# Optimization experiments

Hardware: AMD Instinct MI355X
Metric: run time of the kernel (lower is better)

The kernel has to match this reference:

```python
import jax, jax.numpy as jnp
import numpy as np

B, T, D, H, HS = 4, 1024, 1024, 16, 64  # T == block_size; HS = D // H


def setup_inputs() -> dict:
    key = jax.random.key(0)
    ks = jax.random.split(key, 9)
    s = 0.02
    x = jax.random.normal(ks[0], (B, T, D), dtype=jnp.float32)
    Wk = jax.random.normal(ks[1], (H, D, HS), dtype=jnp.float32) * s
    bk = jax.random.normal(ks[2], (H, HS), dtype=jnp.float32) * s
    Wq = jax.random.normal(ks[3], (H, D, HS), dtype=jnp.float32) * s
    bq = jax.random.normal(ks[4], (H, HS), dtype=jnp.float32) * s
    Wv = jax.random.normal(ks[5], (H, D, HS), dtype=jnp.float32) * s
    bv = jax.random.normal(ks[6], (H, HS), dtype=jnp.float32) * s
    Wp = jax.random.normal(ks[7], (D, D), dtype=jnp.float32) * s
    bp = jax.random.normal(ks[8], (D,), dtype=jnp.float32) * s
    return {"x": x, "Wk": Wk, "bk": bk, "Wq": Wq, "bq": bq,
            "Wv": Wv, "bv": bv, "Wp": Wp, "bp": bp}


def reference(x, Wk, bk, Wq, bq, Wv, bv, Wp, bp):
    Bx, Tx, Dx = x.shape
    # per-head projections, batched over heads: [B,H,T,HS]
    k = jnp.einsum('btd,hde->bhte', x, Wk) + bk[None, :, None, :]
    q = jnp.einsum('btd,hde->bhte', x, Wq) + bq[None, :, None, :]
    v = jnp.einsum('btd,hde->bhte', x, Wv) + bv[None, :, None, :]
    # NOTE: faithful to source: wei = k @ q^T, scaled by C**-0.5 with C=d_model
    scores = jnp.einsum('bhte,bhse->bhts', k, q) * (Dx ** -0.5)
    causal = jnp.tril(jnp.ones((Tx, Tx), dtype=bool))  # tril == 0 masked to -inf
    scores = jnp.where(causal[None, None], scores, -jnp.inf)
    attn = jax.nn.softmax(scores, axis=-1)  # attn_map (dropout is identity in eval)
    out = jnp.einsum('bhts,bhse->bhte', attn, v)
    # concat heads along feature dim (head order preserved)
    out = out.transpose(0, 2, 1, 3).reshape(Bx, Tx, -1)
    out = out @ Wp + bp  # final projection (output dropout identity in eval)
    return (out, attn)
```

## Files before the change

kernel.cpp:

```cpp
#include <hip/hip_runtime.h>
#include <hip/hip_bf16.h>
#include <stdint.h>


using f32x4 = __attribute__((ext_vector_type(4))) float;
using s16x8 = __attribute__((ext_vector_type(8))) short;

#define GLOAD_LDS16(g, l)                                                          \
  __builtin_amdgcn_global_load_lds((const __attribute__((address_space(1))) void*)(g), \
                                   (__attribute__((address_space(3))) void*)(l), 16, 0, 0)

__device__ __forceinline__ unsigned short f2bf(float f) {
  unsigned u = __float_as_uint(f);
  u = (u + 0x7FFFu + ((u >> 16) & 1u)) >> 16;
  return (unsigned short)u;
}

__global__ __launch_bounds__(256) void prep2_kernel(
    const float* __restrict__ x,
    const float* __restrict__ Wk, const float* __restrict__ Wq,
    const float* __restrict__ Wv,
    const float* __restrict__ bk, const float* __restrict__ bq,
    const float* __restrict__ bv,
    const float* __restrict__ Wp,
    unsigned short* __restrict__ xb,
    unsigned short* __restrict__ Wt,
    unsigned short* __restrict__ Wpt,
    float* __restrict__ bqkv) {
  __shared__ float tile[64][65];
  const int bid = blockIdx.x, t = threadIdx.x;

  if (bid < 1024) {
#pragma unroll
    for (int q = 0; q < 4; ++q) {
      int idx = bid * 1024 + q * 256 + t;
      float4 v = ((const float4*)x)[idx];
      ushort4 o;
      o.x = f2bf(v.x); o.y = f2bf(v.y); o.z = f2bf(v.z); o.w = f2bf(v.w);
      ((ushort4*)xb)[idx] = o;
    }
  } else if (bid < 1792) {
    int wb = bid - 1024;
    int p = wb >> 8, rem = wb & 255;
    int h = rem >> 4, dt = rem & 15;
    int d0 = dt * 64;
    const float* Wsrc = (p == 0) ? Wk : (p == 1) ? Wq : Wv;
    const float* src = Wsrc + ((size_t)h * 1024 + d0) * 64;
#pragma unroll
    for (int q = 0; q < 16; ++q) {
      int idx = t + q * 256;
      int dr = idx >> 6, e = idx & 63;
      tile[dr][e] = src[(size_t)dr * 64 + e];
    }
    __syncthreads();
    unsigned short* dst = Wt + ((size_t)p * 1024 + h * 64) * 1024 + d0;
#pragma unroll
    for (int q = 0; q < 16; ++q) {
      int idx = t + q * 256;
      int er = idx >> 6, dc = idx & 63;
      dst[(size_t)er * 1024 + dc] = f2bf(tile[dc][er]);
    }
  } else if (bid < 2048) {
    int wb = bid - 1792;
    int nt = wb >> 4, dt = wb & 15;
    int n0 = nt * 64, d0 = dt * 64;
#pragma unroll
    for (int q = 0; q < 16; ++q) {
      int idx = t + q * 256;
      int dr = idx >> 6, nc = idx & 63;
      tile[dr][nc] = Wp[(size_t)(d0 + dr) * 1024 + n0 + nc];
    }
    __syncthreads();
#pragma unroll
    for (int q = 0; q < 16; ++q) {
      int idx = t + q * 256;
      int er = idx >> 6, dc = idx & 63;
      Wpt[(size_t)(n0 + er) * 1024 + d0 + dc] = f2bf(tile[dc][er]);
    }
  } else {
#pragma unroll
    for (int q = 0; q < 12; ++q) {
      int c = q * 256 + t;
      int p = c >> 10;
      const float* bsrc = (p == 0) ? bk : (p == 1) ? bq : bv;
      bqkv[c] = bsrc[c & 1023];
    }
  }
}

template <int MODE>
__global__ __launch_bounds__(256, 2) void gemm_bt(
    const unsigned short* __restrict__ A,
    const unsigned short* __restrict__ Bt,
    const float* __restrict__ bias,
    unsigned short* __restrict__ kbuf,
    unsigned short* __restrict__ qbuf,
    unsigned short* __restrict__ vtbuf,
    float* __restrict__ fout,
    int gridN) {
  const int K = 1024;
  __shared__ __align__(16) unsigned short As[128 * 64];
  __shared__ __align__(16) unsigned short Bs[128 * 64];

  const int cpx = gridDim.x >> 3;
  const int bid2 = (blockIdx.x & 7) * cpx + (blockIdx.x >> 3);
  const int bm = bid2 / gridN, bn = bid2 % gridN;
  const int tid = threadIdx.x, wave = tid >> 6, lane = tid & 63;
  const int wm = wave >> 1, wn = wave & 1;
  const int l15 = lane & 15, l4 = lane >> 4;
  const long arow0 = (long)bm * 128;
  const long brow0 = (long)bn * 128;

  f32x4 acc[4][4];
  const f32x4 zf4 = {0.f, 0.f, 0.f, 0.f};
#pragma unroll
  for (int i = 0; i < 4; ++i)
#pragma unroll
    for (int j = 0; j < 4; ++j) acc[i][j] = zf4;

  for (int kt = 0; kt < 16; ++kt) {
#pragma unroll
    for (int s = 0; s < 4; ++s) {
      int ob = (wave * 4 + s) * 1024;
      int o = ob + lane * 16;
      int r = o >> 7;
      int cb = (o & 127) ^ ((r & 7) << 4);
      GLOAD_LDS16(A + (arow0 + r) * K + kt * 64 + (cb >> 1), (char*)As + ob);
      GLOAD_LDS16(Bt + (brow0 + r) * K + kt * 64 + (cb >> 1), (char*)Bs + ob);
    }
    __syncthreads();
#pragma unroll
    for (int kk = 0; kk < 2; ++kk) {
      s16x8 af[4], bfv[4];
#pragma unroll
      for (int i = 0; i < 4; ++i) {
        int row = wm * 64 + i * 16 + l15;
        int cb = (kk * 64 + l4 * 16) ^ ((row & 7) << 4);
        af[i] = *(const s16x8*)((const char*)As + row * 128 + cb);
      }
#pragma unroll
      for (int j = 0; j < 4; ++j) {
        int row = wn * 64 + j * 16 + l15;
        int cb = (kk * 64 + l4 * 16) ^ ((row & 7) << 4);
        bfv[j] = *(const s16x8*)((const char*)Bs + row * 128 + cb);
      }
#pragma unroll
      for (int i = 0; i < 4; ++i)
#pragma unroll
        for (int j = 0; j < 4; ++j)
          acc[i][j] = __builtin_amdgcn_mfma_f32_16x16x32_bf16(af[i], bfv[j], acc[i][j], 0, 0, 0);
    }
    __syncthreads();
  }

  const int gc0 = bn * 128;
  if (MODE == 0) {
    const int p = gc0 >> 10;
#pragma unroll
    for (int i = 0; i < 4; ++i) {
      int mrow = (int)arow0 + wm * 64 + i * 16 + l4 * 4;
      int b = mrow >> 10;
      int t = mrow & 1023;
#pragma unroll
      for (int j = 0; j < 4; ++j) {
        int gc = gc0 + wn * 64 + j * 16 + l15;
        int hc = gc & 1023;
        int hh = hc >> 6, e = hc & 63;
        float bb = bias[gc];
#pragma unroll
        for (int r = 0; r < 4; ++r) {
          unsigned short ub = f2bf(acc[i][j][r] + bb);
          if (p == 0)
            kbuf[(((long)(b * 16 + hh)) * 1024 + (t + r)) * 64 + e] = ub;
          else if (p == 1)
            qbuf[(((long)(b * 16 + hh)) * 1024 + (t + r)) * 64 + e] = ub;
          else
            vtbuf[(((long)(b * 16 + hh)) * 64 + e) * 1024 + (t + r)] = ub;
        }
      }
    }
  } else {
#pragma unroll
    for (int i = 0; i < 4; ++i) {
      long mrow = arow0 + wm * 64 + i * 16 + l4 * 4;
#pragma unroll
      for (int j = 0; j < 4; ++j) {
        int gc = gc0 + wn * 64 + j * 16 + l15;
        float bb = bias[gc];
#pragma unroll
        for (int r = 0; r < 4; ++r) fout[(mrow + r) * 1024 + gc] = acc[i][j][r] + bb;
      }
    }
  }
}

__global__ __launch_bounds__(256, 2) void attn_fused(
    const unsigned short* __restrict__ Kb,
    const unsigned short* __restrict__ Qb,
    const unsigned short* __restrict__ Vt,
    float* __restrict__ attn,
    unsigned short* __restrict__ outh) {
  __shared__ __align__(16) unsigned short Ps[128 * 128];
  __shared__ float rsum[2][128];
  __shared__ float rinv[128];

  const int bh = blockIdx.y;
  const int bx = blockIdx.x;
  const int ttile = (bx & 1) ? (7 - (bx >> 1)) : (bx >> 1);
  const int t0 = ttile * 128;
  const int b = bh >> 4, h = bh & 15;
  const unsigned short* Kbh = Kb + (long)bh * 65536;
  const unsigned short* Qbh = Qb + (long)bh * 65536;
  const unsigned short* Vbh = Vt + (long)bh * 65536;
  float* attn_bh = attn + (long)bh * 1048576;

  const int tid = threadIdx.x, wave = tid >> 6, lane = tid & 63;
  const int wm = wave >> 1, wn = wave & 1;
  const int l15 = lane & 15, l4 = lane >> 4;
  const f32x4 zf4 = {0.f, 0.f, 0.f, 0.f};

  s16x8 kf[4][2];
#pragma unroll
  for (int i = 0; i < 4; ++i)
#pragma unroll
    for (int kk = 0; kk < 2; ++kk)
      kf[i][kk] = *(const s16x8*)(Kbh + (long)(t0 + wm * 64 + i * 16 + l15) * 64 + kk * 32 + l4 * 8);

  float rs[4][4];
#pragma unroll
  for (int i = 0; i < 4; ++i)
#pragma unroll
    for (int r = 0; r < 4; ++r) rs[i][r] = 0.f;

  for (int st = 0; st <= ttile; ++st) {
    int s0 = st * 128;
    f32x4 acc[4][4];
#pragma unroll
    for (int i = 0; i < 4; ++i)
#pragma unroll
      for (int j = 0; j < 4; ++j) acc[i][j] = zf4;
#pragma unroll
    for (int kk = 0; kk < 2; ++kk) {
      s16x8 qf[4];
#pragma unroll
      for (int j = 0; j < 4; ++j)
        qf[j] = *(const s16x8*)(Qbh + (long)(s0 + wn * 64 + j * 16 + l15) * 64 + kk * 32 + l4 * 8);
#pragma unroll
      for (int i = 0; i < 4; ++i)
#pragma unroll
        for (int j = 0; j < 4; ++j)
          acc[i][j] = __builtin_amdgcn_mfma_f32_16x16x32_bf16(kf[i][kk], qf[j], acc[i][j], 0, 0, 0);
    }
    bool diag = (st == ttile);
#pragma unroll
    for (int i = 0; i < 4; ++i)
#pragma unroll
      for (int j = 0; j < 4; ++j)
#pragma unroll
        for (int r = 0; r < 4; ++r) {
          float sc = acc[i][j][r] * 0.03125f;
          if (diag) {
            int t = t0 + wm * 64 + i * 16 + l4 * 4 + r;
            int s = s0 + wn * 64 + j * 16 + l15;
            rs[i][r] += (s <= t) ? __expf(sc) : 0.f;
          } else {
            rs[i][r] += __expf(sc);
          }
        }
  }
#pragma unroll
  for (int i = 0; i < 4; ++i)
#pragma unroll
    for (int r = 0; r < 4; ++r) {
      float v = rs[i][r];
      v += __shfl_xor(v, 1);
      v += __shfl_xor(v, 2);
      v += __shfl_xor(v, 4);
      v += __shfl_xor(v, 8);
      if (l15 == 0) rsum[wn][wm * 64 + i * 16 + l4 * 4 + r] = v;
    }
  __syncthreads();
  if (tid < 128) rinv[tid] = 1.0f / (rsum[0][tid] + rsum[1][tid]);
  __syncthreads();

  float rinv_r[4][4];
#pragma unroll
  for (int i = 0; i < 4; ++i)
#pragma unroll
    for (int r = 0; r < 4; ++r) rinv_r[i][r] = rinv[wm * 64 + i * 16 + l4 * 4 + r];

  f32x4 acc2[2][4];
#pragma unroll
  for (int i = 0; i < 2; ++i)
#pragma unroll
    for (int j = 0; j < 4; ++j) acc2[i][j] = zf4;

  for (int st = 0; st < 8; ++st) {
    int s0 = st * 128;
    if (st > ttile) {
      float4 z = make_float4(0.f, 0.f, 0.f, 0.f);
#pragma unroll
      for (int q = 0; q < 16; ++q) {
        int fi = tid + q * 256;
        int row = fi >> 5, c4 = fi & 31;
        *(float4*)(attn_bh + (long)(t0 + row) * 1024 + s0 + c4 * 4) = z;
      }
      continue;
    }
    f32x4 acc[4][4];
#pragma unroll
    for (int i = 0; i < 4; ++i)
#pragma unroll
      for (int j = 0; j < 4; ++j) acc[i][j] = zf4;
#pragma unroll
    for (int kk = 0; kk < 2; ++kk) {
      s16x8 qf[4];
#pragma unroll
      for (int j = 0; j < 4; ++j)
        qf[j] = *(const s16x8*)(Qbh + (long)(s0 + wn * 64 + j * 16 + l15) * 64 + kk * 32 + l4 * 8);
#pragma unroll
      for (int i = 0; i < 4; ++i)
#pragma unroll
        for (int j = 0; j < 4; ++j)
          acc[i][j] = __builtin_amdgcn_mfma_f32_16x16x32_bf16(kf[i][kk], qf[j], acc[i][j], 0, 0, 0);
    }
    bool diag = (st == ttile);
#pragma unroll
    for (int i = 0; i < 4; ++i) {
      int tl = wm * 64 + i * 16 + l4 * 4;
#pragma unroll
      for (int j = 0; j < 4; ++j) {
        int sl = wn * 64 + j * 16 + l15;
#pragma unroll
        for (int r = 0; r < 4; ++r) {
          int t = t0 + tl + r;
          int s = s0 + sl;
          float p = (!diag || s <= t) ? __expf(acc[i][j][r] * 0.03125f) * rinv_r[i][r] : 0.f;
          attn_bh[(long)t * 1024 + s] = p;
          int lt = tl + r;
          Ps[lt * 128 + (sl ^ ((lt & 15) << 3))] = f2bf(p);
        }
      }
    }
    __syncthreads();
#pragma unroll
    for (int kk2 = 0; kk2 < 4; ++kk2) {
      s16x8 pf[2];
#pragma unroll
      for (int i2 = 0; i2 < 2; ++i2) {
        int lt = wave * 32 + i2 * 16 + l15;
        int ls = kk2 * 32 + l4 * 8;
        pf[i2] = *(const s16x8*)&Ps[lt * 128 + (ls ^ ((lt & 15) << 3))];
      }
      s16x8 vf[4];
#pragma unroll
      for (int j2 = 0; j2 < 4; ++j2)
        vf[j2] = *(const s16x8*)(Vbh + (long)(j2 * 16 + l15) * 1024 + s0 + kk2 * 32 + l4 * 8);
#pragma unroll
      for (int i2 = 0; i2 < 2; ++i2)
#pragma unroll
        for (int j2 = 0; j2 < 4; ++j2)
          acc2[i2][j2] = __builtin_amdgcn_mfma_f32_16x16x32_bf16(pf[i2], vf[j2], acc2[i2][j2], 0, 0, 0);
    }
    __syncthreads();
  }

#pragma unroll
  for (int i2 = 0; i2 < 2; ++i2)
#pragma unroll
    for (int j2 = 0; j2 < 4; ++j2)
#pragma unroll
      for (int r = 0; r < 4; ++r) {
        int t = t0 + wave * 32 + i2 * 16 + l4 * 4 + r;
        int e = j2 * 16 + l15;
        outh[(long)(b * 1024 + t) * 1024 + h * 64 + e] = f2bf(acc2[i2][j2][r]);
      }
}

extern "C" void kernel_launch(void* const* d_in, const int* in_sizes, int n_in,
                              void* d_out, int out_size, void* d_ws, size_t ws_size,
                              hipStream_t stream) {
  const float* x  = (const float*)d_in[0];
  const float* Wk = (const float*)d_in[1];
  const float* bk = (const float*)d_in[2];
  const float* Wq = (const float*)d_in[3];
  const float* bq = (const float*)d_in[4];
  const float* Wv = (const float*)d_in[5];
  const float* bv = (const float*)d_in[6];
  const float* Wp = (const float*)d_in[7];
  const float* bp = (const float*)d_in[8];

  char* ws = (char*)d_ws;
  unsigned short* xb   = (unsigned short*)(ws);
  unsigned short* Wt   = (unsigned short*)(ws + 8388608);
  unsigned short* Wpt  = (unsigned short*)(ws + 14680064);
  float*          bqkv = (float*)(ws + 16777216);
  unsigned short* Kbuf = (unsigned short*)(ws + 16789504);
  unsigned short* Qbuf = (unsigned short*)(ws + 25178112);
  unsigned short* Vtb  = (unsigned short*)(ws + 33566720);
  unsigned short* outh = (unsigned short*)(ws + 41955328);

  float* out  = (float*)d_out;
  float* attn = out + 4194304;

  prep2_kernel<<<dim3(2049), dim3(256), 0, stream>>>(x, Wk, Wq, Wv, bk, bq, bv, Wp,
                                                     xb, Wt, Wpt, bqkv);
  gemm_bt<0><<<dim3(768), dim3(256), 0, stream>>>(xb, Wt, bqkv, Kbuf, Qbuf, Vtb,
                                                  (float*)nullptr, 24);
  attn_fused<<<dim3(8, 64), dim3(256), 0, stream>>>(Kbuf, Qbuf, Vtb, attn, outh);
  gemm_bt<1><<<dim3(256), dim3(256), 0, stream>>>(outh, Wpt, bp,
                                                  (unsigned short*)nullptr,
                                                  (unsigned short*)nullptr,
                                                  (unsigned short*)nullptr, out, 8);
}
```

Baseline: 513.4 us.

## Keep full unnormalized probability rows in LDS to avoid recomputing QK in attention

The attention kernel now processes 32-row query tiles and keeps the whole row of exponentiated scores (as bf16) in LDS. This removes the second QK^T pass, which was recomputed only to normalize. The attn matrix is written with coalesced float4 stores scaled by the reciprocal row sum, and normalization of PV is moved to the output. The V projection epilogue also transposes through LDS so that V^T is written with vectorized coalesced stores instead of scattered 2-byte writes. The tradeoff is 64KB of LDS per block, which lowers occupancy. The attn values are also now quantized to bf16 before normalization, which costs some precision.

```diff
diff --git a/kernel.cpp b/kernel.cpp
--- a/kernel.cpp
+++ b/kernel.cpp
@@ -14,6 +14,9 @@
   unsigned u = __float_as_uint(f);
   u = (u + 0x7FFFu + ((u >> 16) & 1u)) >> 16;
   return (unsigned short)u;
+}
+__device__ __forceinline__ float bf2f(unsigned short u) {
+  return __uint_as_float(((unsigned)u) << 16);
 }
 
 __global__ __launch_bounds__(256) void prep2_kernel(
@@ -99,8 +102,9 @@
     float* __restrict__ fout,
     int gridN) {
   const int K = 1024;
-  __shared__ __align__(16) unsigned short As[128 * 64];
-  __shared__ __align__(16) unsigned short Bs[128 * 64];
+  __shared__ __align__(16) unsigned short Sh[128 * 128];
+  unsigned short* As = Sh;
+  unsigned short* Bs = Sh + 8192;
 
   const int cpx = gridDim.x >> 3;
   const int bid2 = (blockIdx.x & 7) * cpx + (blockIdx.x >> 3);
@@ -156,26 +160,52 @@
   const int gc0 = bn * 128;
   if (MODE == 0) {
     const int p = gc0 >> 10;
-#pragma unroll
-    for (int i = 0; i < 4; ++i) {
-      int mrow = (int)arow0 + wm * 64 + i * 16 + l4 * 4;
-      int b = mrow >> 10;
-      int t = mrow & 1023;
-#pragma unroll
-      for (int j = 0; j < 4; ++j) {
-        int gc = gc0 + wn * 64 + j * 16 + l15;
-        int hc = gc & 1023;
-        int hh = hc >> 6, e = hc & 63;
-        float bb = bias[gc];
-#pragma unroll
-        for (int r = 0; r < 4; ++r) {
-          unsigned short ub = f2bf(acc[i][j][r] + bb);
-          if (p == 0)
-            kbuf[(((long)(b * 16 + hh)) * 1024 + (t + r)) * 64 + e] = ub;
-          else if (p == 1)
-            qbuf[(((long)(b * 16 + hh)) * 1024 + (t + r)) * 64 + e] = ub;
-          else
-            vtbuf[(((long)(b * 16 + hh)) * 64 + e) * 1024 + (t + r)] = ub;
+    if (p == 2) {
+#pragma unroll
+      for (int i = 0; i < 4; ++i) {
+        int tl = wm * 64 + i * 16 + l4 * 4;
+#pragma unroll
+        for (int j = 0; j < 4; ++j) {
+          int el = wn * 64 + j * 16 + l15;
+          float bb = bias[gc0 + el];
+#pragma unroll
+          for (int r = 0; r < 4; ++r) {
+            unsigned short ub = f2bf(acc[i][j][r] + bb);
+            *(unsigned short*)((char*)Sh + el * 256 + (((tl + r) * 2) ^ ((el & 15) << 4))) = ub;
+          }
+        }
+      }
+      __syncthreads();
+      const int b = (int)(arow0 >> 10);
+      const int hhb = (gc0 & 1023) >> 6;
+      const int tcb = (int)(arow0 & 1023);
+      int el = tid >> 1, ch = tid & 1;
+      long vrow = ((long)(b * 16 + hhb + (el >> 6))) * 64 + (el & 63);
+#pragma unroll
+      for (int c8 = 0; c8 < 8; ++c8) {
+        s16x8 u = *(const s16x8*)((const char*)Sh + el * 256 + ((ch * 128 + c8 * 16) ^ ((el & 15) << 4)));
+        *(s16x8*)(vtbuf + vrow * 1024 + tcb + ch * 64 + c8 * 8) = u;
+      }
+    } else {
+#pragma unroll
+      for (int i = 0; i < 4; ++i) {
+        int mrow = (int)arow0 + wm * 64 + i * 16 + l4 * 4;
+        int b = mrow >> 10;
+        int t = mrow & 1023;
+#pragma unroll
+        for (int j = 0; j < 4; ++j) {
+          int gc = gc0 + wn * 64 + j * 16 + l15;
+          int hc = gc & 1023;
+          int hh = hc >> 6, e = hc & 63;
+          float bb = bias[gc];
+#pragma unroll
+          for (int r = 0; r < 4; ++r) {
+            unsigned short ub = f2bf(acc[i][j][r] + bb);
+            if (p == 0)
+              kbuf[(((long)(b * 16 + hh)) * 1024 + (t + r)) * 64 + e] = ub;
+            else
+              qbuf[(((long)(b * 16 + hh)) * 1024 + (t + r)) * 64 + e] = ub;
+          }
         }
       }
     }
@@ -194,82 +224,81 @@
   }
 }
 
-__global__ __launch_bounds__(256, 2) void attn_fused(
+__global__ __launch_bounds__(256, 2) void attn_fused2(
     const unsigned short* __restrict__ Kb,
     const unsigned short* __restrict__ Qb,
     const unsigned short* __restrict__ Vt,
     float* __restrict__ attn,
     unsigned short* __restrict__ outh) {
-  __shared__ __align__(16) unsigned short Ps[128 * 128];
-  __shared__ float rsum[2][128];
-  __shared__ float rinv[128];
+  __shared__ __align__(16) unsigned short Pl[32 * 1024];
+  __shared__ float rsum[4][32];
+  __shared__ float rinv[32];
 
   const int bh = blockIdx.y;
   const int bx = blockIdx.x;
-  const int ttile = (bx & 1) ? (7 - (bx >> 1)) : (bx >> 1);
-  const int t0 = ttile * 128;
+  const int ttile = (bx & 1) ? (31 - (bx >> 1)) : (bx >> 1);
+  const int t0 = ttile * 32;
+  const int st_lim = ttile >> 2;
   const int b = bh >> 4, h = bh & 15;
   const unsigned short* Kbh = Kb + (long)bh * 65536;
   const unsigned short* Qbh = Qb + (long)bh * 65536;
   const unsigned short* Vbh = Vt + (long)bh * 65536;
   float* attn_bh = attn + (long)bh * 1048576;
 
-  const int tid = threadIdx.x, wave = tid >> 6, lane = tid & 63;
-  const int wm = wave >> 1, wn = wave & 1;
+  const int tid = threadIdx.x, w = tid >> 6, lane = tid & 63;
   const int l15 = lane & 15, l4 = lane >> 4;
   const f32x4 zf4 = {0.f, 0.f, 0.f, 0.f};
 
-  s16x8 kf[4][2];
-#pragma unroll
-  for (int i = 0; i < 4; ++i)
+  s16x8 kf[2][2];
+#pragma unroll
+  for (int i = 0; i < 2; ++i)
 #pragma unroll
     for (int kk = 0; kk < 2; ++kk)
-      kf[i][kk] = *(const s16x8*)(Kbh + (long)(t0 + wm * 64 + i * 16 + l15) * 64 + kk * 32 + l4 * 8);
-
-  float rs[4][4];
-#pragma unroll
-  for (int i = 0; i < 4; ++i)
+      kf[i][kk] = *(const s16x8*)(Kbh + (long)(t0 + i * 16 + l15) * 64 + kk * 32 + l4 * 8);
+
+  float rs[2][4];
+#pragma unroll
+  for (int i = 0; i < 2; ++i)
 #pragma unroll
     for (int r = 0; r < 4; ++r) rs[i][r] = 0.f;
 
-  for (int st = 0; st <= ttile; ++st) {
+  for (int st = 0; st <= st_lim; ++st) {
     int s0 = st * 128;
-    f32x4 acc[4][4];
-#pragma unroll
-    for (int i = 0; i < 4; ++i)
-#pragma unroll
-      for (int j = 0; j < 4; ++j) acc[i][j] = zf4;
+    f32x4 acc[2][2];
+#pragma unroll
+    for (int i = 0; i < 2; ++i)
+#pragma unroll
+      for (int j = 0; j < 2; ++j) acc[i][j] = zf4;
 #pragma unroll
     for (int kk = 0; kk < 2; ++kk) {
-      s16x8 qf[4];
-#pragma unroll
-      for (int j = 0; j < 4; ++j)
-        qf[j] = *(const s16x8*)(Qbh + (long)(s0 + wn * 64 + j * 16 + l15) * 64 + kk * 32 + l4 * 8);
-#pragma unroll
-      for (int i = 0; i < 4; ++i)
-#pragma unroll
-        for (int j = 0; j < 4; ++j)
+      s16x8 qf[2];
+#pragma unroll
+      for (int j = 0; j < 2; ++j)
+        qf[j] = *(const s16x8*)(Qbh + (long)(s0 + w * 32 + j * 16 + l15) * 64 + kk * 32 + l4 * 8);
+#pragma unroll
+      for (int i = 0; i < 2; ++i)
+#pragma unroll
+        for (int j = 0; j < 2; ++j)
           acc[i][j] = __builtin_amdgcn_mfma_f32_16x16x32_bf16(kf[i][kk], qf[j], acc[i][j], 0, 0, 0);
     }
-    bool diag = (st == ttile);
-#pragma unroll
-    for (int i = 0; i < 4; ++i)
-#pragma unroll
-      for (int j = 0; j < 4; ++j)
+    bool diag = (st == st_lim);
+#pragma unroll
+    for (int i = 0; i < 2; ++i)
+#pragma unroll
+      for (int j = 0; j < 2; ++j) {
+        int s = s0 + w * 32 + j * 16 + l15;
 #pragma unroll
         for (int r = 0; r < 4; ++r) {
-          float sc = acc[i][j][r] * 0.03125f;
-          if (diag) {
-            int t = t0 + wm * 64 + i * 16 + l4 * 4 + r;
-            int s = s0 + wn * 64 + j * 16 + l15;
-            rs[i][r] += (s <= t) ? __expf(sc) : 0.f;
-          } else {
-            rs[i][r] += __expf(sc);
-          }
+          int tl = i * 16 + l4 * 4 + r;
+          float e = __expf(acc[i][j][r] * 0.03125f);
+          unsigned short ub = (!diag || s <= t0 + tl) ? f2bf(e) : (unsigned short)0;
+          rs[i][r] += bf2f(ub);
+          *(unsigned short*)((char*)Pl + tl * 2048 + ((s * 2) ^ ((tl & 7) << 4))) = ub;
         }
-  }
-#pragma unroll
-  for (int i = 0; i < 4; ++i)
+      }
+  }
+#pragma unroll
+  for (int i = 0; i < 2; ++i)
 #pragma unroll
     for (int r = 0; r < 4; ++r) {
       float v = rs[i][r];
@@ -277,104 +306,65 @@
       v += __shfl_xor(v, 2);
       v += __shfl_xor(v, 4);
       v += __shfl_xor(v, 8);
-      if (l15 == 0) rsum[wn][wm * 64 + i * 16 + l4 * 4 + r] = v;
+      if (l15 == 0) rsum[w][i * 16 + l4 * 4 + r] = v;
     }
   __syncthreads();
-  if (tid < 128) rinv[tid] = 1.0f / (rsum[0][tid] + rsum[1][tid]);
+  if (tid < 32) rinv[tid] = 1.0f / (rsum[0][tid] + rsum[1][tid] + rsum[2][tid] + rsum[3][tid]);
   __syncthreads();
 
-  float rinv_r[4][4];
-#pragma unroll
-  for (int i = 0; i < 4; ++i)
-#pragma unroll
-    for (int r = 0; r < 4; ++r) rinv_r[i][r] = rinv[wm * 64 + i * 16 + l4 * 4 + r];
-
-  f32x4 acc2[2][4];
-#pragma unroll
-  for (int i = 0; i < 2; ++i)
-#pragma unroll
-    for (int j = 0; j < 4; ++j) acc2[i][j] = zf4;
-
-  for (int st = 0; st < 8; ++st) {
+  {
+    int row = tid >> 3, cb = tid & 7;
+    int tg = t0 + row;
+    float ri = rinv[row];
+#pragma unroll
+    for (int g = 0; g < 16; ++g) {
+      int c0 = g * 64 + cb * 8;
+      float4 o0, o1;
+      if ((g >> 1) <= st_lim) {
+        s16x8 u = *(const s16x8*)((const char*)Pl + row * 2048 + ((c0 * 2) ^ ((row & 7) << 4)));
+        o0.x = bf2f((unsigned short)u[0]) * ri;
+        o0.y = bf2f((unsigned short)u[1]) * ri;
+        o0.z = bf2f((unsigned short)u[2]) * ri;
+        o0.w = bf2f((unsigned short)u[3]) * ri;
+        o1.x = bf2f((unsigned short)u[4]) * ri;
+        o1.y = bf2f((unsigned short)u[5]) * ri;
+        o1.z = bf2f((unsigned short)u[6]) * ri;
+        o1.w = bf2f((unsigned short)u[7]) * ri;
+      } else {
+        o0 = make_float4(0.f, 0.f, 0.f, 0.f);
+        o1 = o0;
+      }
+      *(float4*)(attn_bh + (long)tg * 1024 + c0) = o0;
+      *(float4*)(attn_bh + (long)tg * 1024 + c0 + 4) = o1;
+    }
+  }
+
+  f32x4 acc2[2];
+  acc2[0] = zf4; acc2[1] = zf4;
+  const int i2 = w & 1, eh = (w >> 1) * 32;
+  for (int st = 0; st <= st_lim; ++st) {
     int s0 = st * 128;
-    if (st > ttile) {
-      float4 z = make_float4(0.f, 0.f, 0.f, 0.f);
-#pragma unroll
-      for (int q = 0; q < 16; ++q) {
-        int fi = tid + q * 256;
-        int row = fi >> 5, c4 = fi & 31;
-        *(float4*)(attn_bh + (long)(t0 + row) * 1024 + s0 + c4 * 4) = z;
-      }
-      continue;
-    }
-    f32x4 acc[4][4];
-#pragma unroll
-    for (int i = 0; i < 4; ++i)
-#pragma unroll
-      for (int j = 0; j < 4; ++j) acc[i][j] = zf4;
-#pragma unroll
-    for (int kk = 0; kk < 2; ++kk) {
-      s16x8 qf[4];
-#pragma unroll
-      for (int j = 0; j < 4; ++j)
-        qf[j] = *(const s16x8*)(Qbh + (long)(s0 + wn * 64 + j * 16 + l15) * 64 + kk * 32 + l4 * 8);
-#pragma unroll
-      for (int i = 0; i < 4; ++i)
-#pragma unroll
-        for (int j = 0; j < 4; ++j)
-          acc[i][j] = __builtin_amdgcn_mfma_f32_16x16x32_bf16(kf[i][kk], qf[j], acc[i][j], 0, 0, 0);
-    }
-    bool diag = (st == ttile);
-#pragma unroll
-    for (int i = 0; i < 4; ++i) {
-      int tl = wm * 64 + i * 16 + l4 * 4;
-#pragma unroll
-      for (int j = 0; j < 4; ++j) {
-        int sl = wn * 64 + j * 16 + l15;
-#pragma unroll
-        for (int r = 0; r < 4; ++r) {
-          int t = t0 + tl + r;
-          int s = s0 + sl;
-          float p = (!diag || s <= t) ? __expf(acc[i][j][r] * 0.03125f) * rinv_r[i][r] : 0.f;
-          attn_bh[(long)t * 1024 + s] = p;
-          int lt = tl + r;
-          Ps[lt * 128 + (sl ^ ((lt & 15) << 3))] = f2bf(p);
-        }
-      }
-    }
-    __syncthreads();
 #pragma unroll
     for (int kk2 = 0; kk2 < 4; ++kk2) {
-      s16x8 pf[2];
-#pragma unroll
-      for (int i2 = 0; i2 < 2; ++i2) {
-        int lt = wave * 32 + i2 * 16 + l15;
-        int ls = kk2 * 32 + l4 * 8;
-        pf[i2] = *(const s16x8*)&Ps[lt * 128 + (ls ^ ((lt & 15) << 3))];
-      }
-      s16x8 vf[4];
-#pragma unroll
-      for (int j2 = 0; j2 < 4; ++j2)
-        vf[j2] = *(const s16x8*)(Vbh + (long)(j2 * 16 + l15) * 1024 + s0 + kk2 * 32 + l4 * 8);
-#pragma unroll
-      for (int i2 = 0; i2 < 2; ++i2)
-#pragma unroll
-        for (int j2 = 0; j2 < 4; ++j2)
-          acc2[i2][j2] = __builtin_amdgcn_mfma_f32_16x16x32_bf16(pf[i2], vf[j2], acc2[i2][j2], 0, 0, 0);
-    }
-    __syncthreads();
-  }
-
-#pragma unroll
-  for (int i2 = 0; i2 < 2; ++i2)
-#pragma unroll
-    for (int j2 = 0; j2 < 4; ++j2)
-#pragma unroll
-      for (int r = 0; r < 4; ++r) {
-        int t = t0 + wave * 32 + i2 * 16 + l4 * 4 + r;
-        int e = j2 * 16 + l15;
-        outh[(long)(b * 1024 + t) * 1024 + h * 64 + e] = f2bf(acc2[i2][j2][r]);
-      }
+      int tl = i2 * 16 + l15;
+      int k = s0 + kk2 * 32 + l4 * 8;
+      s16x8 pf = *(const s16x8*)((const char*)Pl + tl * 2048 + ((k * 2) ^ ((tl & 7) << 4)));
+#pragma unroll
+      for (int j2 = 0; j2 < 2; ++j2) {
+        s16x8 vf = *(const s16x8*)(Vbh + (long)(eh + j2 * 16 + l15) * 1024 + k);
+        acc2[j2] = __builtin_amdgcn_mfma_f32_16x16x32_bf16(pf, vf, acc2[j2], 0, 0, 0);
+      }
+    }
+  }
+#pragma unroll
+  for (int j2 = 0; j2 < 2; ++j2)
+#pragma unroll
+    for (int r = 0; r < 4; ++r) {
+      int tl = i2 * 16 + l4 * 4 + r;
+      int e = eh + j2 * 16 + l15;
+      float o = acc2[j2][r] * rinv[tl];
+      outh[(long)(b * 1024 + t0 + tl) * 1024 + h * 64 + e] = f2bf(o);
+    }
 }
 
 extern "C" void kernel_launch(void* const* d_in, const int* in_sizes, int n_in,
@@ -407,7 +397,7 @@
                                                      xb, Wt, Wpt, bqkv);
   gemm_bt<0><<<dim3(768), dim3(256), 0, stream>>>(xb, Wt, bqkv, Kbuf, Qbuf, Vtb,
                                                   (float*)nullptr, 24);
-  attn_fused<<<dim3(8, 64), dim3(256), 0, stream>>>(Kbuf, Qbuf, Vtb, attn, outh);
+  attn_fused2<<<dim3(32, 64), dim3(256), 0, stream>>>(Kbuf, Qbuf, Vtb, attn, outh);
   gemm_bt<1><<<dim3(256), dim3(256), 0, stream>>>(outh, Wpt, bp,
                                                   (unsigned short*)nullptr,
                                                   (unsigned short*)nullptr,
```

New measurement: 443.7 us. -13.6%, faster.
